# Optimization experiments

Hardware: AMD Instinct MI355X
Metric: run time of the kernel (lower is better)

The kernel has to match this reference:

```python
import jax, jax.numpy as jnp
import numpy as np

N_NODES = 100000
N_EDGES = 3200000
N_GRAPHS = 512
IN_CH = 128
HID = 32
OUT = 2


def setup_inputs() -> dict:
    key = jax.random.key(0)
    ks = jax.random.split(key, 6)
    x = jax.random.normal(ks[0], (N_NODES, IN_CH), dtype=jnp.float32)
    edge_index = jax.random.randint(ks[1], (2, N_EDGES), 0, N_NODES, dtype=jnp.int64)
    batch = jnp.sort(jax.random.randint(ks[2], (N_NODES,), 0, N_GRAPHS, dtype=jnp.int64))
    # Glorot-ish params
    W1 = jax.random.normal(ks[3], (IN_CH, HID), dtype=jnp.float32) * (1.0 / np.sqrt(IN_CH))
    b1 = jnp.zeros((HID,), dtype=jnp.float32)
    W2 = jax.random.normal(ks[4], (HID, HID), dtype=jnp.float32) * (1.0 / np.sqrt(HID))
    b2 = jnp.zeros((HID,), dtype=jnp.float32)
    Wl = jax.random.normal(ks[5], (HID, OUT), dtype=jnp.float32) * (1.0 / np.sqrt(HID))
    bl = jnp.zeros((OUT,), dtype=jnp.float32)
    return {"x": x, "edge_index": edge_index, "batch": batch,
            "W1": W1, "b1": b1, "W2": W2, "b2": b2, "Wl": Wl, "bl": bl}


def _gcn_conv(h, src, dst, W, b, n_nodes):
    # PyG GCNConv: transform, add self-loops, symmetric deg normalization,
    # scatter-add messages from src -> dst, then bias.
    h = h @ W  # [N, F_out]
    ones = jnp.ones(src.shape[0], dtype=h.dtype)
    # degree on target nodes, +1 for the implicit self-loop
    deg = jax.ops.segment_sum(ones, dst, num_segments=n_nodes) + 1.0
    dinv = jax.lax.rsqrt(deg)  # deg >= 1 always
    norm = dinv[src] * dinv[dst]  # [E]
    agg = jax.ops.segment_sum(h[src] * norm[:, None], dst, num_segments=n_nodes)
    # self-loop contribution: norm_ii = dinv_i^2
    agg = agg + h * (dinv * dinv)[:, None]
    return agg + b


def reference(x, edge_index, batch, W1, b1, W2, b2, Wl, bl):
    n_nodes = x.shape[0]
    src, dst = edge_index[0], edge_index[1]
    h = jax.nn.relu(_gcn_conv(x, src, dst, W1, b1, n_nodes))
    h = jax.nn.relu(_gcn_conv(h, src, dst, W2, b2, n_nodes))
    # global mean pool per graph
    sums = jax.ops.segment_sum(h, batch, num_segments=N_GRAPHS)
    counts = jax.ops.segment_sum(jnp.ones(n_nodes, h.dtype), batch, num_segments=N_GRAPHS)
    pooled = sums / jnp.maximum(counts, 1.0)[:, None]  # [G, 32]
    return pooled @ Wl + bl  # [G, 2]
```

## Files before the change

### kernel.cpp

```cpp
#include <hip/hip_runtime.h>
#include <hip/hip_bf16.h>

#define N_NODES 100000
#define N_EDGES 3200000
#define N_GRAPHS 512
#define NBUK 782
#define CAP 4608
#define CCAP 5632
#define FILL_CHUNK 8192
#define FILL_BLOCKS ((N_EDGES + FILL_CHUNK - 1) / FILL_CHUNK)
#define GEMM1_BLOCKS ((N_NODES + 63) / 64)

__device__ __forceinline__ float blo(unsigned v) { return __uint_as_float(v << 16); }
__device__ __forceinline__ float bhi(unsigned v) { return __uint_as_float(v & 0xffff0000u); }

__global__ __launch_bounds__(1024) void k_fatA(const int* __restrict__ ei,
                                               int* __restrict__ gcnt,
                                               unsigned* __restrict__ packed,
                                               const float* __restrict__ x,
                                               const float* __restrict__ W1,
                                               float* __restrict__ H1u) {
    __shared__ __align__(16) char smem[49152];
    int t = threadIdx.x;
    if (blockIdx.x < FILL_BLOCKS) {
        unsigned* buf = (unsigned*)smem;
        int* h    = (int*)(smem + 32768);
        int* base = (int*)(smem + 35896);
        int* sb   = (int*)(smem + 39024);
        int* ws   = (int*)(smem + 42152);
        for (int i = t; i < NBUK; i += 1024) h[i] = 0;
        __syncthreads();
        int s0 = blockIdx.x * FILL_CHUNK;
        int ng = min(FILL_CHUNK, N_EDGES - s0) >> 2;
        const int4* src4 = (const int4*)(ei + s0);
        const int4* dst4 = (const int4*)(ei + N_EDGES + s0);
        int4 sv[2], dv[2];
        int  rk[2][4];
#pragma unroll
        for (int g = 0; g < 2; g++) {
            int gi = t + g * 1024;
            if (gi < ng) {
                sv[g] = src4[gi];
                dv[g] = dst4[gi];
                rk[g][0] = atomicAdd(&h[dv[g].x >> 7], 1);
                rk[g][1] = atomicAdd(&h[dv[g].y >> 7], 1);
                rk[g][2] = atomicAdd(&h[dv[g].z >> 7], 1);
                rk[g][3] = atomicAdd(&h[dv[g].w >> 7], 1);
            }
        }
        __syncthreads();
        for (int i = t; i < NBUK; i += 1024) {
            int c = h[i];
            base[i] = c ? atomicAdd(&gcnt[i], c) : 0;
        }
        int lane = t & 63, wv = t >> 6;
        int hval = (t < NBUK) ? h[t] : 0;
        int v = hval;
#pragma unroll
        for (int d2 = 1; d2 < 64; d2 <<= 1) {
            int o = __shfl_up(v, d2);
            if (lane >= d2) v += o;
        }
        if (lane == 63) ws[wv] = v;
        __syncthreads();
        if (wv == 0) {
            int s = (lane < 16) ? ws[lane] : 0;
            int sv2 = s;
#pragma unroll
            for (int d2 = 1; d2 < 16; d2 <<= 1) {
                int o = __shfl_up(sv2, d2);
                if (lane >= d2) sv2 += o;
            }
            if (lane < 16) ws[lane] = sv2 - s;
        }
        __syncthreads();
        if (t < NBUK) sb[t] = v + ws[wv] - hval;
        __syncthreads();
#pragma unroll
        for (int g = 0; g < 2; g++) {
            int gi = t + g * 1024;
            if (gi < ng) {
                int s[4] = {sv[g].x, sv[g].y, sv[g].z, sv[g].w};
                int d[4] = {dv[g].x, dv[g].y, dv[g].z, dv[g].w};
#pragma unroll
                for (int k = 0; k < 4; k++) {
                    int bk = d[k] >> 7;
                    buf[sb[bk] + rk[g][k]] = (unsigned)s[k] | (((unsigned)d[k] & 127u) << 17);
                }
            }
        }
        __syncthreads();
        int g16 = t >> 4;
        int l16 = t & 15;
        for (int bk = g16; bk < NBUK; bk += 64) {
            int c = h[bk];
            if (!c) continue;
            unsigned* gp = packed + (size_t)bk * CAP + base[bk];
            int lb = sb[bk];
            for (int j = l16; j < c; j += 16) gp[j] = buf[lb + j];
        }
    } else {
        float* Ws = (float*)smem;
        float* xs = (float*)(smem + 16384);
        int b = blockIdx.x - FILL_BLOCKS;
        ((float4*)Ws)[t] = ((const float4*)W1)[t];
        int row0 = b * 64;
        const float4* x4 = (const float4*)(x + (size_t)row0 * 128);
        float4* xs4 = (float4*)xs;
        int maxr = min(64, N_NODES - row0);
        int nf4 = maxr * 32;
#pragma unroll
        for (int i = 0; i < 8; i++) {
            int idx = t + i * 1024;
            if (idx < nf4) xs4[idx] = x4[idx];
        }
        __syncthreads();
        int col = t & 31;
        int g = t >> 5;
        int r0 = 2 * g, r1 = 2 * g + 1;
        const float4* xa4 = xs4 + r0 * 32;
        const float4* xb4 = xs4 + r1 * 32;
        float a0 = 0.f, a1 = 0.f;
#pragma unroll 8
        for (int k4 = 0; k4 < 32; k4++) {
            float4 xa = xa4[k4];
            float4 xb = xb4[k4];
            float w0 = Ws[(k4 * 4 + 0) * 32 + col];
            float w1 = Ws[(k4 * 4 + 1) * 32 + col];
            float w2 = Ws[(k4 * 4 + 2) * 32 + col];
            float w3 = Ws[(k4 * 4 + 3) * 32 + col];
            a0 += xa.x * w0 + xa.y * w1 + xa.z * w2 + xa.w * w3;
            a1 += xb.x * w0 + xb.y * w1 + xb.z * w2 + xb.w * w3;
        }
        if (row0 + r0 < N_NODES) H1u[(size_t)(row0 + r0) * 32 + col] = a0;
        if (row0 + r1 < N_NODES) H1u[(size_t)(row0 + r1) * 32 + col] = a1;
    }
}

__global__ __launch_bounds__(512) void k_csr(const unsigned* __restrict__ packed,
                                             const int* __restrict__ gcnt,
                                             int* __restrict__ rp, int* __restrict__ rpe,
                                             float* __restrict__ dinv,
                                             int* __restrict__ csr,
                                             const float* __restrict__ H1u,
                                             __hip_bfloat16* __restrict__ H1s) {
    __shared__ int deg4[4][128];
    __shared__ int nb0[128];
    __shared__ float dsh[128];
    __shared__ int wsum0;
    __shared__ int ntot;
    __shared__ int lcsr[CCAP] __attribute__((aligned(16)));
    int t = threadIdx.x;
    int b = blockIdx.x;
    deg4[t >> 7][t & 127] = 0;
    __syncthreads();
    int n = gcnt[b];
    const unsigned* pb = packed + (size_t)b * CAP;
    int cp = t >> 7;
    unsigned pv[3][4];
    int rk[3][4];
#pragma unroll
    for (int g = 0; g < 3; g++) {
        int i0 = 4 * (t + g * 512);
        if (i0 < n) {
            if (i0 + 3 < n) {
                uint4 p = *(const uint4*)(pb + i0);
                pv[g][0] = p.x; pv[g][1] = p.y; pv[g][2] = p.z; pv[g][3] = p.w;
            } else {
#pragma unroll
                for (int k = 0; k < 4; k++) pv[g][k] = (i0 + k < n) ? pb[i0 + k] : 0u;
            }
#pragma unroll
            for (int k = 0; k < 4; k++)
                if (i0 + k < n) rk[g][k] = atomicAdd(&deg4[cp][pv[g][k] >> 17], 1);
        }
    }
    __syncthreads();
    int lane = t & 63;
    int d = 0, e1 = 0, e2 = 0, e3 = 0;
    if (t < 128) {
        int c0 = deg4[0][t], c1 = deg4[1][t], c2 = deg4[2][t], c3 = deg4[3][t];
        e1 = c0; e2 = c0 + c1; e3 = e2 + c2; d = e3 + c3;
    }
    int p16 = (d + 15) & ~15;
    int v = (t < 128) ? p16 : 0;
#pragma unroll
    for (int d2 = 1; d2 < 64; d2 <<= 1) {
        int o = __shfl_up(v, d2);
        if (lane >= d2) v += o;
    }
    if (t == 63) wsum0 = v;
    __syncthreads();
    if (t < 128) {
        deg4[0][t] = 0; deg4[1][t] = e1; deg4[2][t] = e2; deg4[3][t] = e3;
        int inc = v + ((t >= 64) ? wsum0 : 0);
        int l0 = inc - p16;
        nb0[t] = l0;
        float di = rsqrtf((float)d + 1.0f);
        dsh[t] = di;
        int node = b * 128 + t;
        if (node < N_NODES) {
            rp[node] = b * CCAP + l0;
            rpe[node] = b * CCAP + l0 + p16;
            dinv[node] = di;
        }
        for (int j = d; j < p16; j++) lcsr[l0 + j] = N_NODES;
        if (t == 127) ntot = l0 + p16;
    }
    __syncthreads();
#pragma unroll
    for (int g = 0; g < 3; g++) {
        int i0 = 4 * (t + g * 512);
        if (i0 < n) {
#pragma unroll
            for (int k = 0; k < 4; k++) {
                if (i0 + k < n) {
                    unsigned p = pv[g][k];
                    int dst = p >> 17;
                    lcsr[nb0[dst] + deg4[cp][dst] + rk[g][k]] = (int)(p & 0x1FFFFu);
                }
            }
        }
    }
    __syncthreads();
    int nq = (ntot + 3) >> 2;
    int4* dst4 = (int4*)(csr + (size_t)b * CCAP);
    const int4* sl4 = (const int4*)lcsr;
    for (int i = t; i < nq; i += 512) dst4[i] = sl4[i];
    for (int i = t; i < 1024; i += 512) {
        int row = i >> 3, q = i & 7;
        int node = b * 128 + row;
        if (node < N_NODES) {
            float4 fv = ((const float4*)H1u)[(size_t)node * 8 + q];
            float di = dsh[row];
            __hip_bfloat16 tmp[4];
            tmp[0] = __float2bfloat16(fv.x * di);
            tmp[1] = __float2bfloat16(fv.y * di);
            tmp[2] = __float2bfloat16(fv.z * di);
            tmp[3] = __float2bfloat16(fv.w * di);
            *(uint2*)(H1s + (size_t)node * 32 + q * 4) = *(uint2*)tmp;
        }
    }
    if (b == 0 && t < 16) ((unsigned*)(H1s + (size_t)N_NODES * 32))[t] = 0u;
}

__global__ void k_gather(const __hip_bfloat16* __restrict__ Hs, const float* __restrict__ dinv,
                         const int* __restrict__ rp, const int* __restrict__ rpe,
                         const int* __restrict__ csr,
                         const float* __restrict__ bias, float* __restrict__ hout) {
    int lane = threadIdx.x & 63;
    int fb = lane & 3;
    int qn = lane >> 4;
    int wave = (blockIdx.x * 256 + threadIdx.x) >> 6;
    int wid = wave * 4 + qn;
    const uint4* H4 = (const uint4*)Hs;
    int beg = rp[wid];
    int pdeg = rpe[wid] - beg;
    int grp = lane & 48;
    int es = (lane >> 2) & 3;
    int es4 = es * 4;
    float a0=0.f,a1=0.f,a2=0.f,a3=0.f,a4=0.f,a5=0.f,a6=0.f,a7=0.f;
    int e = 0;
    for (; e + 32 <= pdeg; e += 32) {
        int2 cv2 = *(const int2*)(csr + beg + e + 2 * (lane & 15));
#pragma unroll
        for (int k = 0; k < 8; k++) {
            int src = __shfl((k & 1) ? cv2.y : cv2.x, grp | (es4 + (k >> 1)));
            uint4 v = H4[(unsigned)src * 4u + fb];
            a0 += blo(v.x); a1 += bhi(v.x);
            a2 += blo(v.y); a3 += bhi(v.y);
            a4 += blo(v.z); a5 += bhi(v.z);
            a6 += blo(v.w); a7 += bhi(v.w);
        }
    }
    if (e < pdeg) {
        int cv = csr[beg + e + (lane & 15)];
#pragma unroll
        for (int k = 0; k < 4; k++) {
            int src = __shfl(cv, grp | (es + 4 * k));
            uint4 v = H4[(unsigned)src * 4u + fb];
            a0 += blo(v.x); a1 += bhi(v.x);
            a2 += blo(v.y); a3 += bhi(v.y);
            a4 += blo(v.z); a5 += bhi(v.z);
            a6 += blo(v.w); a7 += bhi(v.w);
        }
    }
#pragma unroll
    for (int m = 4; m <= 8; m <<= 1) {
        a0 += __shfl_xor(a0, m); a1 += __shfl_xor(a1, m);
        a2 += __shfl_xor(a2, m); a3 += __shfl_xor(a3, m);
        a4 += __shfl_xor(a4, m); a5 += __shfl_xor(a5, m);
        a6 += __shfl_xor(a6, m); a7 += __shfl_xor(a7, m);
    }
    if (es == 0) {
        float di = dinv[wid];
        uint4 vw = H4[(unsigned)wid * 4u + fb];
        float4 bA = *(const float4*)(bias + fb * 8);
        float4 bB = *(const float4*)(bias + fb * 8 + 4);
        float4 oA, oB;
        oA.x = fmaxf((a0 + blo(vw.x)) * di + bA.x, 0.f);
        oA.y = fmaxf((a1 + bhi(vw.x)) * di + bA.y, 0.f);
        oA.z = fmaxf((a2 + blo(vw.y)) * di + bA.z, 0.f);
        oA.w = fmaxf((a3 + bhi(vw.y)) * di + bA.w, 0.f);
        oB.x = fmaxf((a4 + blo(vw.z)) * di + bB.x, 0.f);
        oB.y = fmaxf((a5 + bhi(vw.z)) * di + bB.y, 0.f);
        oB.z = fmaxf((a6 + blo(vw.w)) * di + bB.z, 0.f);
        oB.w = fmaxf((a7 + bhi(vw.w)) * di + bB.w, 0.f);
        float* o = hout + (size_t)wid * 32 + fb * 8;
        *(float4*)o = oA;
        *(float4*)(o + 4) = oB;
    }
}

__global__ void k_gemm2(const float* __restrict__ h1, const float* __restrict__ W2,
                        const float* __restrict__ dinv, __hip_bfloat16* __restrict__ H2s) {
    __shared__ float Ws[32 * 32];
    __shared__ float xs[32 * 32];
    int t = threadIdx.x;
    ((float4*)Ws)[t] = ((const float4*)W2)[t];
    int row0 = blockIdx.x * 32;
    ((float4*)xs)[t] = ((const float4*)(h1 + (size_t)row0 * 32))[t];
    __syncthreads();
    int col = t & 31;
    int rb = (t >> 5) * 4;
    float a0 = 0.f, a1 = 0.f, a2 = 0.f, a3 = 0.f;
#pragma unroll
    for (int k = 0; k < 32; k++) {
        float w = Ws[k * 32 + col];
        a0 += xs[(rb + 0) * 32 + k] * w;
        a1 += xs[(rb + 1) * 32 + k] * w;
        a2 += xs[(rb + 2) * 32 + k] * w;
        a3 += xs[(rb + 3) * 32 + k] * w;
    }
    int r = row0 + rb;
    __hip_bfloat16* o = H2s + (size_t)r * 32 + col;
    o[0]  = __float2bfloat16(a0 * dinv[r + 0]);
    o[32] = __float2bfloat16(a1 * dinv[r + 1]);
    o[64] = __float2bfloat16(a2 * dinv[r + 2]);
    o[96] = __float2bfloat16(a3 * dinv[r + 3]);
    if (blockIdx.x == 0 && t < 16) ((unsigned*)(H2s + (size_t)N_NODES * 32))[t] = 0u;
}

__global__ __launch_bounds__(256) void k_pool(const float* __restrict__ h2,
                                              const int* __restrict__ batch,
                                              const float* __restrict__ Wl,
                                              const float* __restrict__ bl,
                                              float* __restrict__ out) {
    __shared__ float red[256];
    __shared__ float pooled[32];
    int g = blockIdx.x;
    int t = threadIdx.x;
    int lo = 0, hi = N_NODES;
    while (lo < hi) { int m = (lo + hi) >> 1; if (batch[m] < g) lo = m + 1; else hi = m; }
    int s = lo;
    hi = N_NODES;
    while (lo < hi) { int m = (lo + hi) >> 1; if (batch[m] < g + 1) lo = m + 1; else hi = m; }
    int e = lo;
    int f = t & 31, r0 = t >> 5;
    float acc = 0.f;
    for (int r = s + r0; r < e; r += 8) acc += h2[(size_t)r * 32 + f];
    red[t] = acc;
    __syncthreads();
    for (int off = 128; off >= 32; off >>= 1) {
        if (t < off) red[t] += red[t + off];
        __syncthreads();
    }
    if (t < 32) pooled[t] = red[t] / fmaxf((float)(e - s), 1.0f);
    __syncthreads();
    if (t < 2) {
        float a = bl[t];
#pragma unroll
        for (int k = 0; k < 32; k++) a += pooled[k] * Wl[k * 2 + t];
        out[g * 2 + t] = a;
    }
}

extern "C" void kernel_launch(void* const* d_in, const int* in_sizes, int n_in,
                              void* d_out, int out_size, void* d_ws, size_t ws_size,
                              hipStream_t stream) {
    const float* x    = (const float*)d_in[0];
    const int*   ei   = (const int*)d_in[1];
    const int*   batch= (const int*)d_in[2];
    const float* W1   = (const float*)d_in[3];
    const float* b1   = (const float*)d_in[4];
    const float* W2   = (const float*)d_in[5];
    const float* b2   = (const float*)d_in[6];
    const float* Wl   = (const float*)d_in[7];
    const float* bl   = (const float*)d_in[8];
    float* out = (float*)d_out;

    char* w = (char*)d_ws;
    size_t off = 0;
    auto take = [&](size_t bytes) -> char* {
        char* p = w + off;
        off = (off + bytes + 255) & ~(size_t)255;
        return p;
    };
    __hip_bfloat16* H1s = (__hip_bfloat16*)take((size_t)(N_NODES + 1) * 32 * 2);
    float*          h1  = (float*)take((size_t)N_NODES * 32 * 4);
    char*           shared = take((size_t)NBUK * CAP * 4);
    unsigned*       packed = (unsigned*)shared;
    __hip_bfloat16* H2s    = (__hip_bfloat16*)shared;
    int*      csr    = (int*)  take((size_t)NBUK * CCAP * 4 + 1024);
    float*    dinv   = (float*)take((size_t)N_NODES * 4);
    int*      rp     = (int*)  take((size_t)N_NODES * 4);
    int*      rpe    = (int*)  take((size_t)N_NODES * 4);
    int*      gcnt   = (int*)  take((size_t)NBUK * 4);

    hipMemsetAsync(gcnt, 0, (size_t)NBUK * 4, stream);

    k_fatA  <<<FILL_BLOCKS + GEMM1_BLOCKS, 1024, 0, stream>>>(ei, gcnt, packed, x, W1, h1);
    k_csr   <<<NBUK, 512, 0, stream>>>(packed, gcnt, rp, rpe, dinv, csr, h1, H1s);
    k_gather<<<N_NODES / 16, 256, 0, stream>>>(H1s, dinv, rp, rpe, csr, b1, h1);
    k_gemm2 <<<N_NODES / 32, 256, 0, stream>>>(h1, W2, dinv, H2s);
    k_gather<<<N_NODES / 16, 256, 0, stream>>>(H2s, dinv, rp, rpe, csr, b2, h1);
    k_pool  <<<N_GRAPHS, 256, 0, stream>>>(h1, batch, Wl, bl, out);
}
```

Before: 248.3 us.

## Assign 8 lanes per node in gather kernel instead of 16

The gather kernel now processes 8 destination nodes per wavefront, each with 8 lanes (4 feature slices × 2 edge slots), instead of 4 nodes with 16 lanes. Each lane issues two independent row loads per step over 16-edge chunks, and only one xor-shuffle reduction stage remains. The grid is halved to match. This is meant to cut lane waste on padded-degree tails and reduce the reduction overhead, at the cost of less edge parallelism per node and an assumption that CSR rows are padded to multiples of 16.

```diff
diff --git a/kernel.cpp b/kernel.cpp
--- a/kernel.cpp
+++ b/kernel.cpp
@@ -250,49 +250,36 @@
                          const float* __restrict__ bias, float* __restrict__ hout) {
     int lane = threadIdx.x & 63;
     int fb = lane & 3;
-    int qn = lane >> 4;
+    int es2 = (lane >> 2) & 1;
+    int qn = lane >> 3;
     int wave = (blockIdx.x * 256 + threadIdx.x) >> 6;
-    int wid = wave * 4 + qn;
+    int wid = wave * 8 + qn;
     const uint4* H4 = (const uint4*)Hs;
     int beg = rp[wid];
     int pdeg = rpe[wid] - beg;
-    int grp = lane & 48;
-    int es = (lane >> 2) & 3;
-    int es4 = es * 4;
+    int grp8 = lane & 56;
+    int k0 = es2 * 4;
     float a0=0.f,a1=0.f,a2=0.f,a3=0.f,a4=0.f,a5=0.f,a6=0.f,a7=0.f;
-    int e = 0;
-    for (; e + 32 <= pdeg; e += 32) {
-        int2 cv2 = *(const int2*)(csr + beg + e + 2 * (lane & 15));
-#pragma unroll
-        for (int k = 0; k < 8; k++) {
-            int src = __shfl((k & 1) ? cv2.y : cv2.x, grp | (es4 + (k >> 1)));
-            uint4 v = H4[(unsigned)src * 4u + fb];
-            a0 += blo(v.x); a1 += bhi(v.x);
-            a2 += blo(v.y); a3 += bhi(v.y);
-            a4 += blo(v.z); a5 += bhi(v.z);
-            a6 += blo(v.w); a7 += bhi(v.w);
-        }
-    }
-    if (e < pdeg) {
-        int cv = csr[beg + e + (lane & 15)];
-#pragma unroll
-        for (int k = 0; k < 4; k++) {
-            int src = __shfl(cv, grp | (es + 4 * k));
-            uint4 v = H4[(unsigned)src * 4u + fb];
-            a0 += blo(v.x); a1 += bhi(v.x);
-            a2 += blo(v.y); a3 += bhi(v.y);
-            a4 += blo(v.z); a5 += bhi(v.z);
-            a6 += blo(v.w); a7 += bhi(v.w);
-        }
-    }
-#pragma unroll
-    for (int m = 4; m <= 8; m <<= 1) {
-        a0 += __shfl_xor(a0, m); a1 += __shfl_xor(a1, m);
-        a2 += __shfl_xor(a2, m); a3 += __shfl_xor(a3, m);
-        a4 += __shfl_xor(a4, m); a5 += __shfl_xor(a5, m);
-        a6 += __shfl_xor(a6, m); a7 += __shfl_xor(a7, m);
-    }
-    if (es == 0) {
+    for (int e = 0; e < pdeg; e += 16) {
+        int2 cv2 = *(const int2*)(csr + beg + e + 2 * (lane & 7));
+#pragma unroll
+        for (int kk = 0; kk < 4; kk++) {
+            int k = k0 + kk;
+            int sa = __shfl(cv2.x, grp8 | k);
+            int sb = __shfl(cv2.y, grp8 | k);
+            uint4 va = H4[(unsigned)sa * 4u + fb];
+            uint4 vb = H4[(unsigned)sb * 4u + fb];
+            a0 += blo(va.x) + blo(vb.x); a1 += bhi(va.x) + bhi(vb.x);
+            a2 += blo(va.y) + blo(vb.y); a3 += bhi(va.y) + bhi(vb.y);
+            a4 += blo(va.z) + blo(vb.z); a5 += bhi(va.z) + bhi(vb.z);
+            a6 += blo(va.w) + blo(vb.w); a7 += bhi(va.w) + bhi(vb.w);
+        }
+    }
+    a0 += __shfl_xor(a0, 4); a1 += __shfl_xor(a1, 4);
+    a2 += __shfl_xor(a2, 4); a3 += __shfl_xor(a3, 4);
+    a4 += __shfl_xor(a4, 4); a5 += __shfl_xor(a5, 4);
+    a6 += __shfl_xor(a6, 4); a7 += __shfl_xor(a7, 4);
+    if (es2 == 0) {
         float di = dinv[wid];
         uint4 vw = H4[(unsigned)wid * 4u + fb];
         float4 bA = *(const float4*)(bias + fb * 8);
@@ -411,8 +398,8 @@
 
     k_fatA  <<<FILL_BLOCKS + GEMM1_BLOCKS, 1024, 0, stream>>>(ei, gcnt, packed, x, W1, h1);
     k_csr   <<<NBUK, 512, 0, stream>>>(packed, gcnt, rp, rpe, dinv, csr, h1, H1s);
-    k_gather<<<N_NODES / 16, 256, 0, stream>>>(H1s, dinv, rp, rpe, csr, b1, h1);
+    k_gather<<<N_NODES / 32, 256, 0, stream>>>(H1s, dinv, rp, rpe, csr, b1, h1);
     k_gemm2 <<<N_NODES / 32, 256, 0, stream>>>(h1, W2, dinv, H2s);
-    k_gather<<<N_NODES / 16, 256, 0, stream>>>(H2s, dinv, rp, rpe, csr, b2, h1);
+    k_gather<<<N_NODES / 32, 256, 0, stream>>>(H2s, dinv, rp, rpe, csr, b2, h1);
     k_pool  <<<N_GRAPHS, 256, 0, stream>>>(h1, batch, Wl, bl, out);
 }
```

Result: no change. 250.4 us (+0.8%).
